# Optimization experiments

Hardware: AMD Instinct MI355X
Metric: run time of the kernel (lower is better)

The kernel has to match this reference:

```python
import jax, jax.numpy as jnp
import numpy as np

B, LQ, LK, D, DV = 8, 2048, 2048, 128, 128


def setup_inputs() -> dict:
    key = jax.random.key(0)
    ks = jax.random.split(key, 6)
    return {
        "query": jax.random.normal(ks[0], (B, LQ, D), dtype=jnp.float32),
        "key": jax.random.normal(ks[1], (B, LK, D), dtype=jnp.float32),
        "value": jax.random.normal(ks[2], (B, LK, DV), dtype=jnp.float32),
        "Wq": jax.random.normal(ks[3], (D, D), dtype=jnp.float32) * 0.08,
        "Wk": jax.random.normal(ks[4], (D, D), dtype=jnp.float32) * 0.08,
        "Wv": jax.random.normal(ks[5], (DV, DV), dtype=jnp.float32) * 0.08,
        "attention_mask": jnp.ones((B, 1, LK), dtype=jnp.int32),
    }


def reference(query, key, value, Wq, Wk, Wv, attention_mask):
    # Linear projections (right-multiplication, as in `x @ W`)
    q = query @ Wq          # [B, lq, n_ed]
    k = key @ Wk            # [B, lk, n_ed]
    v = value @ Wv          # [B, lk, n_ev]
    scale = 1.0 / np.sqrt(q.shape[-1])
    scores = jnp.einsum("bqd,bkd->bqk", q, k) * scale  # [B, lq, lk]
    # additive mask: 0 where attend, -inf where mask==0 (broadcasts)
    mask_vals = jnp.where(attention_mask == 0, -jnp.inf, 0.0).astype(scores.dtype)
    scores = scores + mask_vals
    attn = jax.nn.softmax(scores, axis=-1)
    return attn @ v         # [B, lq, n_ev]
```

## Files before the change

kernel.cpp:

```cpp
#include <hip/hip_runtime.h>
#include <hip/hip_bf16.h>

typedef unsigned short u16;
typedef unsigned int u32;
typedef __attribute__((ext_vector_type(8))) short s8v;
typedef __attribute__((ext_vector_type(4))) float f4v;

#define B_N 8
#define L_Q 2048
#define L_K 2048
#define DIM 128
#define KT  64
#define KSPLIT 4
#define KCHUNK (L_K / KSPLIT)

__device__ __forceinline__ u16 f2bf(float f) {
  union { float f; unsigned u; } v; v.f = f;
  return (u16)((v.u + 0x7fffu + ((v.u >> 16) & 1u)) >> 16);
}
__device__ __forceinline__ u32 packbf2(float a, float b) {
  union { __hip_bfloat162 h; u32 u; } v;
  v.h = __float22bfloat162_rn(make_float2(a, b));
  return v.u;
}

__global__ __launch_bounds__(256) void proj_mfma(
    const float* __restrict__ query, const float* __restrict__ key,
    const float* __restrict__ value, const float* __restrict__ Wq,
    const float* __restrict__ Wk, const float* __restrict__ Wv,
    u16* __restrict__ qp, u16* __restrict__ kp, u16* __restrict__ vt) {
  __shared__ __align__(16) u16 Wt[DIM][DIM + 8];
  __shared__ __align__(16) u16 Vt[DIM][KT + 8];
  const int tid = threadIdx.x;
  const int bi = blockIdx.x;
  const int which = bi >> 8;
  const int sub = bi & 255;
  const int b = sub >> 5;
  const int rt = sub & 31;
  const float* X = (which == 0) ? query : (which == 1) ? key : value;
  const float* W = (which == 0) ? Wq : (which == 1) ? Wk : Wv;
  const float wscale = (which == 0) ? (1.44269504089f / 11.3137084990f) : 1.0f;

#pragma unroll
  for (int i = 0; i < 16; ++i) {
    int f4i = tid + i * 256;
    float4 w4 = *(const float4*)(W + f4i * 4);
    int row = f4i >> 5, col = (f4i & 31) * 4;
    Wt[col + 0][row] = f2bf(w4.x * wscale);
    Wt[col + 1][row] = f2bf(w4.y * wscale);
    Wt[col + 2][row] = f2bf(w4.z * wscale);
    Wt[col + 3][row] = f2bf(w4.w * wscale);
  }
  __syncthreads();

  const int w = tid >> 6, lane = tid & 63;
  const int ln = lane & 15, quad = lane >> 4;
  const int xrow = rt * 64 + w * 16 + ln;
  const float* Xr = X + ((size_t)b * L_Q + xrow) * DIM;

  s8v a[4];
#pragma unroll
  for (int ks = 0; ks < 4; ++ks) {
    float4 xa = *(const float4*)(Xr + ks * 32 + quad * 8);
    float4 xb = *(const float4*)(Xr + ks * 32 + quad * 8 + 4);
    s8v t;
    t[0] = (short)f2bf(xa.x); t[1] = (short)f2bf(xa.y);
    t[2] = (short)f2bf(xa.z); t[3] = (short)f2bf(xa.w);
    t[4] = (short)f2bf(xb.x); t[5] = (short)f2bf(xb.y);
    t[6] = (short)f2bf(xb.z); t[7] = (short)f2bf(xb.w);
    a[ks] = t;
  }

  f4v acc[8];
#pragma unroll
  for (int i = 0; i < 8; ++i) acc[i] = (f4v){0.f, 0.f, 0.f, 0.f};
#pragma unroll
  for (int ks = 0; ks < 4; ++ks)
#pragma unroll
    for (int nt = 0; nt < 8; ++nt) {
      s8v bw = *(const s8v*)&Wt[nt * 16 + ln][ks * 32 + quad * 8];
      acc[nt] = __builtin_amdgcn_mfma_f32_16x16x32_bf16(a[ks], bw, acc[nt], 0, 0, 0);
    }

  if (which < 2) {
    u16* Y = ((which == 0) ? qp : kp) + ((size_t)b * L_Q + rt * 64 + w * 16) * DIM;
#pragma unroll
    for (int nt = 0; nt < 8; ++nt)
#pragma unroll
      for (int r = 0; r < 4; ++r)
        Y[(size_t)(quad * 4 + r) * DIM + nt * 16 + ln] = f2bf(acc[nt][r]);
  } else {
#pragma unroll
    for (int nt = 0; nt < 8; ++nt) {
      *(u32*)&Vt[nt * 16 + ln][w * 16 + quad * 4]     = packbf2(acc[nt][0], acc[nt][1]);
      *(u32*)&Vt[nt * 16 + ln][w * 16 + quad * 4 + 2] = packbf2(acc[nt][2], acc[nt][3]);
    }
    __syncthreads();
    u16* Y = vt + (size_t)b * DIM * L_K;
#pragma unroll
    for (int r = 0; r < 4; ++r) {
      int c = tid + r * 256;
      int row = c >> 3, cc = (c & 7) * 8;
      *(s8v*)(Y + (size_t)row * L_K + rt * 64 + cc) = *(const s8v*)&Vt[row][cc];
    }
  }
}

__global__ __launch_bounds__(256, 4) void flash_split(
    const u16* __restrict__ qp, const u16* __restrict__ kp,
    const u16* __restrict__ vt, const int* __restrict__ mask,
    float* __restrict__ po, float* __restrict__ ml) {
  __shared__ __align__(16) u16 Kl[KT][DIM + 8];
  __shared__ __align__(16) u16 Vl[DIM][KT + 8];
  __shared__ float biasl[KT];

  const int tid = threadIdx.x;
  const int bi = blockIdx.x;
  const int b = bi & 7;
  const int rest = bi >> 3;
  const int p = rest & 3;
  const int q0 = (rest >> 2) * 64;
  const int w = tid >> 6;
  const int lane = tid & 63;
  const int ln = lane & 15;
  const int quad = lane >> 4;
  const int kbase = p * KCHUNK;

  const u16* Qb = qp + (size_t)b * L_Q * DIM;
  const u16* Kb = kp + (size_t)b * L_K * DIM;
  const u16* Vb = vt + (size_t)b * DIM * L_K;
  const int* mb = mask + b * L_K;
  u16* Pw = ((u16*)Kl) + w * (16 * 72);

  s8v aq[4];
  const int qrow = q0 + w * 16 + ln;
#pragma unroll
  for (int ks = 0; ks < 4; ++ks)
    aq[ks] = *(const s8v*)(Qb + (size_t)qrow * DIM + ks * 32 + quad * 8);

  f4v o[8];
#pragma unroll
  for (int i = 0; i < 8; ++i) o[i] = (f4v){0.f, 0.f, 0.f, 0.f};
  float mrow = -__builtin_inff();
  float lrow = 0.f;

  for (int it = 0; it < KCHUNK / KT; ++it) {
    const int k0 = kbase + it * KT;
#pragma unroll
    for (int r = 0; r < 4; ++r) {
      int c16 = tid + r * 256;
      int row = c16 >> 4, cc = (c16 & 15) * 8;
      *(s8v*)&Kl[row][cc] = *(const s8v*)(Kb + (size_t)(k0 + row) * DIM + cc);
    }
#pragma unroll
    for (int r = 0; r < 4; ++r) {
      int c16 = tid + r * 256;
      int row = c16 >> 3, cc = (c16 & 7) * 8;
      *(s8v*)&Vl[row][cc] = *(const s8v*)(Vb + (size_t)row * L_K + k0 + cc);
    }
    if (tid < KT) biasl[tid] = (mb[k0 + tid] == 0) ? -__builtin_inff() : 0.f;
    __syncthreads();

    f4v s[4];
#pragma unroll
    for (int mt = 0; mt < 4; ++mt) s[mt] = (f4v){0.f, 0.f, 0.f, 0.f};
#pragma unroll
    for (int ks = 0; ks < 4; ++ks)
#pragma unroll
      for (int mt = 0; mt < 4; ++mt) {
        s8v bk = *(const s8v*)&Kl[mt * 16 + ln][ks * 32 + quad * 8];
        s[mt] = __builtin_amdgcn_mfma_f32_16x16x32_bf16(bk, aq[ks], s[mt], 0, 0, 0);
      }
#pragma unroll
    for (int mt = 0; mt < 4; ++mt) {
      float4 bt = *(const float4*)&biasl[mt * 16 + quad * 4];
      s[mt][0] += bt.x; s[mt][1] += bt.y; s[mt][2] += bt.z; s[mt][3] += bt.w;
    }
    float m16 = s[0][0];
#pragma unroll
    for (int mt = 0; mt < 4; ++mt)
#pragma unroll
      for (int r = 0; r < 4; ++r) m16 = fmaxf(m16, s[mt][r]);
    m16 = fmaxf(m16, __shfl_xor(m16, 16, 64));
    m16 = fmaxf(m16, __shfl_xor(m16, 32, 64));

    float mn = fmaxf(mrow, m16);
    float alpha = exp2f(fminf(mrow - mn, 0.f));
    mrow = mn;
    float rs = 0.f;
#pragma unroll
    for (int mt = 0; mt < 4; ++mt)
#pragma unroll
      for (int r = 0; r < 4; ++r) {
        s[mt][r] = exp2f(fminf(s[mt][r] - mn, 0.f));
        rs += s[mt][r];
      }
    rs += __shfl_xor(rs, 16, 64);
    rs += __shfl_xor(rs, 32, 64);
    lrow = lrow * alpha + rs;

    __syncthreads();

#pragma unroll
    for (int mt = 0; mt < 4; ++mt) {
      *(u32*)(Pw + ln * 72 + mt * 16 + quad * 4)     = packbf2(s[mt][0], s[mt][1]);
      *(u32*)(Pw + ln * 72 + mt * 16 + quad * 4 + 2) = packbf2(s[mt][2], s[mt][3]);
    }

    float ar[4];
#pragma unroll
    for (int r = 0; r < 4; ++r) ar[r] = __shfl(alpha, quad * 4 + r, 64);
#pragma unroll
    for (int n2 = 0; n2 < 8; ++n2)
#pragma unroll
      for (int r = 0; r < 4; ++r) o[n2][r] *= ar[r];

#pragma unroll
    for (int kv = 0; kv < 2; ++kv) {
      s8v ap = *(const s8v*)(Pw + ln * 72 + kv * 32 + quad * 8);
#pragma unroll
      for (int n2 = 0; n2 < 8; ++n2) {
        s8v bv = *(const s8v*)&Vl[n2 * 16 + ln][kv * 32 + quad * 8];
        o[n2] = __builtin_amdgcn_mfma_f32_16x16x32_bf16(ap, bv, o[n2], 0, 0, 0);
      }
    }
    __syncthreads();
  }

#pragma unroll
  for (int n2 = 0; n2 < 8; ++n2)
#pragma unroll
    for (int r = 0; r < 4; ++r) {
      size_t q = (size_t)b * L_Q + q0 + w * 16 + quad * 4 + r;
      po[(q * KSPLIT + p) * DIM + n2 * 16 + ln] = o[n2][r];
    }
  if (quad == 0) {
    size_t q = (size_t)b * L_Q + q0 + w * 16 + ln;
    *(float2*)&ml[(q * KSPLIT + p) * 2] = make_float2(mrow, lrow);
  }
}

__global__ __launch_bounds__(256) void combine(
    const float* __restrict__ po, const float* __restrict__ ml,
    float* __restrict__ out) {
  const int t = threadIdx.x;
  const int lr = t >> 5, l32 = t & 31;
  const size_t q = (size_t)blockIdx.x * 8 + lr;

  float m[KSPLIT], l[KSPLIT];
#pragma unroll
  for (int p = 0; p < KSPLIT; ++p) {
    m[p] = ml[(q * KSPLIT + p) * 2 + 0];
    l[p] = ml[(q * KSPLIT + p) * 2 + 1];
  }
  float M = m[0];
#pragma unroll
  for (int p = 1; p < KSPLIT; ++p) M = fmaxf(M, m[p]);
  float wp[KSPLIT], L = 0.f;
#pragma unroll
  for (int p = 0; p < KSPLIT; ++p) {
    wp[p] = exp2f(fminf(m[p] - M, 0.f));
    L += l[p] * wp[p];
  }
  float invL = 1.0f / L;

  float4 acc = make_float4(0.f, 0.f, 0.f, 0.f);
#pragma unroll
  for (int p = 0; p < KSPLIT; ++p) {
    float4 v = *(const float4*)(po + (q * KSPLIT + p) * DIM + l32 * 4);
    acc.x += wp[p] * v.x; acc.y += wp[p] * v.y;
    acc.z += wp[p] * v.z; acc.w += wp[p] * v.w;
  }
  acc.x *= invL; acc.y *= invL; acc.z *= invL; acc.w *= invL;
  *(float4*)(out + q * DIM + l32 * 4) = acc;
}

extern "C" void kernel_launch(void* const* d_in, const int* in_sizes, int n_in,
                              void* d_out, int out_size, void* d_ws, size_t ws_size,
                              hipStream_t stream) {
  const float* query = (const float*)d_in[0];
  const float* key   = (const float*)d_in[1];
  const float* value = (const float*)d_in[2];
  const float* Wq    = (const float*)d_in[3];
  const float* Wk    = (const float*)d_in[4];
  const float* Wv    = (const float*)d_in[5];
  const int*   mask  = (const int*)d_in[6];
  float* out = (float*)d_out;

  u16* qp = (u16*)d_ws;
  u16* kp = qp + (size_t)B_N * L_Q * DIM;
  u16* vt = kp + (size_t)B_N * L_K * DIM;
  float* po = (float*)(vt + (size_t)B_N * DIM * L_K);
  float* ml = po + (size_t)B_N * L_Q * KSPLIT * DIM;

  hipLaunchKernelGGL(proj_mfma, dim3(768), dim3(256), 0, stream,
                     query, key, value, Wq, Wk, Wv, qp, kp, vt);
  hipLaunchKernelGGL(flash_split, dim3(1024), dim3(256), 0, stream,
                     qp, kp, vt, mask, po, ml);
  hipLaunchKernelGGL(combine, dim3((B_N * L_Q) / 8), dim3(256), 0, stream,
                     po, ml, out);
}
```

Measured before the change: 141.7 us.

## Store Q/K/V in MFMA fragment-major layout and load K/V tiles via async LDS DMA

The projection kernel now writes Q, K and V in a fragment-major tiled layout, so each MFMA operand is a contiguous 512-element block that can be read with lane*8 offsets. The flash kernel then loads K and V tiles straight into LDS with global_load_lds, skipping the register round trip and the padded row layout. It also skips the mask bias add when a wavefront ballot shows the whole tile is unmasked, and it uses the raw hardware exp2 intrinsic. In exchange the layouts are tightly coupled across the kernels, and the unpadded LDS layout could bring bank conflicts.

```diff
diff --git a/kernel.cpp b/kernel.cpp
--- a/kernel.cpp
+++ b/kernel.cpp
@@ -23,14 +23,20 @@
   v.h = __float22bfloat162_rn(make_float2(a, b));
   return v.u;
 }
+__device__ __forceinline__ void async16(const u16* g, u16* l) {
+  __builtin_amdgcn_global_load_lds(
+      (const __attribute__((address_space(1))) u32*)(const void*)g,
+      (__attribute__((address_space(3))) u32*)(void*)l, 16, 0, 0);
+}
+
 
 __global__ __launch_bounds__(256) void proj_mfma(
     const float* __restrict__ query, const float* __restrict__ key,
     const float* __restrict__ value, const float* __restrict__ Wq,
     const float* __restrict__ Wk, const float* __restrict__ Wv,
-    u16* __restrict__ qp, u16* __restrict__ kp, u16* __restrict__ vt) {
-  __shared__ __align__(16) u16 Wt[DIM][DIM + 8];
-  __shared__ __align__(16) u16 Vt[DIM][KT + 8];
+    u16* __restrict__ qp, u16* __restrict__ kp, u16* __restrict__ vp) {
+  __shared__ __align__(16) u16 Wf[32 * 520];
+  __shared__ __align__(16) u16 Fb[8192];
   const int tid = threadIdx.x;
   const int bi = blockIdx.x;
   const int which = bi >> 8;
@@ -45,11 +51,14 @@
   for (int i = 0; i < 16; ++i) {
     int f4i = tid + i * 256;
     float4 w4 = *(const float4*)(W + f4i * 4);
-    int row = f4i >> 5, col = (f4i & 31) * 4;
-    Wt[col + 0][row] = f2bf(w4.x * wscale);
-    Wt[col + 1][row] = f2bf(w4.y * wscale);
-    Wt[col + 2][row] = f2bf(w4.z * wscale);
-    Wt[col + 3][row] = f2bf(w4.w * wscale);
+    int k = f4i >> 5, col = (f4i & 31) * 4;
+    int ks = k >> 5, qd = (k & 31) >> 3, j = k & 7;
+    float wv[4] = {w4.x, w4.y, w4.z, w4.w};
+#pragma unroll
+    for (int c = 0; c < 4; ++c) {
+      int n = col + c;
+      Wf[(ks * 8 + (n >> 4)) * 520 + (qd * 16 + (n & 15)) * 8 + j] = f2bf(wv[c] * wscale);
+    }
   }
   __syncthreads();
 
@@ -74,44 +83,55 @@
   f4v acc[8];
 #pragma unroll
   for (int i = 0; i < 8; ++i) acc[i] = (f4v){0.f, 0.f, 0.f, 0.f};
+  const u16* Wl0 = Wf + lane * 8;
 #pragma unroll
   for (int ks = 0; ks < 4; ++ks)
 #pragma unroll
     for (int nt = 0; nt < 8; ++nt) {
-      s8v bw = *(const s8v*)&Wt[nt * 16 + ln][ks * 32 + quad * 8];
+      s8v bw = *(const s8v*)(Wl0 + (ks * 8 + nt) * 520);
       acc[nt] = __builtin_amdgcn_mfma_f32_16x16x32_bf16(a[ks], bw, acc[nt], 0, 0, 0);
     }
 
   if (which < 2) {
-    u16* Y = ((which == 0) ? qp : kp) + ((size_t)b * L_Q + rt * 64 + w * 16) * DIM;
-#pragma unroll
-    for (int nt = 0; nt < 8; ++nt)
+#pragma unroll
+    for (int nt = 0; nt < 8; ++nt) {
+      int ks = nt >> 1;
+      int f = (which == 0) ? (w * 4 + ks) : (ks * 4 + w);
+      int lp = ((nt & 1) * 2 + (ln >> 3)) * 16;
+      int j = ln & 7;
 #pragma unroll
       for (int r = 0; r < 4; ++r)
-        Y[(size_t)(quad * 4 + r) * DIM + nt * 16 + ln] = f2bf(acc[nt][r]);
+        Fb[f * 512 + (lp + quad * 4 + r) * 8 + j] = f2bf(acc[nt][r]);
+    }
   } else {
 #pragma unroll
     for (int nt = 0; nt < 8; ++nt) {
-      *(u32*)&Vt[nt * 16 + ln][w * 16 + quad * 4]     = packbf2(acc[nt][0], acc[nt][1]);
-      *(u32*)&Vt[nt * 16 + ln][w * 16 + quad * 4 + 2] = packbf2(acc[nt][2], acc[nt][3]);
-    }
-    __syncthreads();
-    u16* Y = vt + (size_t)b * DIM * L_K;
-#pragma unroll
-    for (int r = 0; r < 4; ++r) {
-      int c = tid + r * 256;
-      int row = c >> 3, cc = (c & 7) * 8;
-      *(s8v*)(Y + (size_t)row * L_K + rt * 64 + cc) = *(const s8v*)&Vt[row][cc];
-    }
+      int f = (w >> 1) * 8 + nt;
+      int lp = ((w & 1) * 2 + (quad >> 1)) * 16 + ln;
+      int jb = (quad & 1) * 4;
+#pragma unroll
+      for (int r = 0; r < 4; ++r)
+        Fb[f * 512 + lp * 8 + jb + r] = f2bf(acc[nt][r]);
+    }
+  }
+  __syncthreads();
+
+  u16* Y = (which == 0) ? qp + (size_t)(b * 512 + rt * 16) * 512
+         : (which == 1) ? kp + (size_t)((b * 32 + rt) * 16) * 512
+                        : vp + (size_t)((b * 32 + rt) * 16) * 512;
+#pragma unroll
+  for (int r = 0; r < 4; ++r) {
+    int c = tid + r * 256;
+    *(s8v*)(Y + c * 8) = *(const s8v*)(Fb + c * 8);
   }
 }
 
 __global__ __launch_bounds__(256, 4) void flash_split(
     const u16* __restrict__ qp, const u16* __restrict__ kp,
-    const u16* __restrict__ vt, const int* __restrict__ mask,
+    const u16* __restrict__ vp, const int* __restrict__ mask,
     float* __restrict__ po, float* __restrict__ ml) {
-  __shared__ __align__(16) u16 Kl[KT][DIM + 8];
-  __shared__ __align__(16) u16 Vl[DIM][KT + 8];
+  __shared__ __align__(16) u16 Kf[8192];
+  __shared__ __align__(16) u16 Vf[8192];
   __shared__ float biasl[KT];
 
   const int tid = threadIdx.x;
@@ -119,24 +139,19 @@
   const int b = bi & 7;
   const int rest = bi >> 3;
   const int p = rest & 3;
-  const int q0 = (rest >> 2) * 64;
+  const int qb = rest >> 2;
   const int w = tid >> 6;
   const int lane = tid & 63;
   const int ln = lane & 15;
   const int quad = lane >> 4;
-  const int kbase = p * KCHUNK;
-
-  const u16* Qb = qp + (size_t)b * L_Q * DIM;
-  const u16* Kb = kp + (size_t)b * L_K * DIM;
-  const u16* Vb = vt + (size_t)b * DIM * L_K;
+
   const int* mb = mask + b * L_K;
-  u16* Pw = ((u16*)Kl) + w * (16 * 72);
-
+
+  const u16* Qt = qp + ((size_t)(b * 128 + qb * 4 + w) * 4) * 512;
   s8v aq[4];
-  const int qrow = q0 + w * 16 + ln;
 #pragma unroll
   for (int ks = 0; ks < 4; ++ks)
-    aq[ks] = *(const s8v*)(Qb + (size_t)qrow * DIM + ks * 32 + quad * 8);
+    aq[ks] = *(const s8v*)(Qt + ks * 512 + lane * 8);
 
   f4v o[8];
 #pragma unroll
@@ -144,21 +159,25 @@
   float mrow = -__builtin_inff();
   float lrow = 0.f;
 
+  const u16* Kl0 = Kf + lane * 8;
+  const u16* Vl0 = Vf + lane * 8;
+  u16* Pw = Kf + w * 1024;
+  const u16* Pl0 = Pw + lane * 8;
+
   for (int it = 0; it < KCHUNK / KT; ++it) {
-    const int k0 = kbase + it * KT;
-#pragma unroll
-    for (int r = 0; r < 4; ++r) {
-      int c16 = tid + r * 256;
-      int row = c16 >> 4, cc = (c16 & 15) * 8;
-      *(s8v*)&Kl[row][cc] = *(const s8v*)(Kb + (size_t)(k0 + row) * DIM + cc);
-    }
-#pragma unroll
-    for (int r = 0; r < 4; ++r) {
-      int c16 = tid + r * 256;
-      int row = c16 >> 3, cc = (c16 & 7) * 8;
-      *(s8v*)&Vl[row][cc] = *(const s8v*)(Vb + (size_t)row * L_K + k0 + cc);
-    }
-    if (tid < KT) biasl[tid] = (mb[k0 + tid] == 0) ? -__builtin_inff() : 0.f;
+    const int kt = p * (KCHUNK / KT) + it;
+    const int k0 = kt * KT;
+    const u16* Ktile = kp + (size_t)((b * 32 + kt) * 16) * 512;
+    const u16* Vtile = vp + (size_t)((b * 32 + kt) * 16) * 512;
+#pragma unroll
+    for (int c = 0; c < 4; ++c) {
+      int cg = w * 4 + c;
+      async16(Ktile + (size_t)(cg * 64 + lane) * 8, Kf + cg * 512);
+      async16(Vtile + (size_t)(cg * 64 + lane) * 8, Vf + cg * 512);
+    }
+    int mv = mb[k0 + lane];
+    bool allones = (__ballot(mv != 0) == ~0ull);
+    if (!allones && tid < KT) biasl[tid] = (mv == 0) ? -__builtin_inff() : 0.f;
     __syncthreads();
 
     f4v s[4];
@@ -168,13 +187,15 @@
     for (int ks = 0; ks < 4; ++ks)
 #pragma unroll
       for (int mt = 0; mt < 4; ++mt) {
-        s8v bk = *(const s8v*)&Kl[mt * 16 + ln][ks * 32 + quad * 8];
+        s8v bk = *(const s8v*)(Kl0 + (ks * 4 + mt) * 512);
         s[mt] = __builtin_amdgcn_mfma_f32_16x16x32_bf16(bk, aq[ks], s[mt], 0, 0, 0);
       }
-#pragma unroll
-    for (int mt = 0; mt < 4; ++mt) {
-      float4 bt = *(const float4*)&biasl[mt * 16 + quad * 4];
-      s[mt][0] += bt.x; s[mt][1] += bt.y; s[mt][2] += bt.z; s[mt][3] += bt.w;
+    if (!allones) {
+#pragma unroll
+      for (int mt = 0; mt < 4; ++mt) {
+        float4 bt = *(const float4*)&biasl[mt * 16 + quad * 4];
+        s[mt][0] += bt.x; s[mt][1] += bt.y; s[mt][2] += bt.z; s[mt][3] += bt.w;
+      }
     }
     float m16 = s[0][0];
 #pragma unroll
@@ -185,14 +206,14 @@
     m16 = fmaxf(m16, __shfl_xor(m16, 32, 64));
 
     float mn = fmaxf(mrow, m16);
-    float alpha = exp2f(fminf(mrow - mn, 0.f));
+    float alpha = __builtin_amdgcn_exp2f(fminf(mrow - mn, 0.f));
     mrow = mn;
     float rs = 0.f;
 #pragma unroll
     for (int mt = 0; mt < 4; ++mt)
 #pragma unroll
       for (int r = 0; r < 4; ++r) {
-        s[mt][r] = exp2f(fminf(s[mt][r] - mn, 0.f));
+        s[mt][r] = __builtin_amdgcn_exp2f(fminf(s[mt][r] - mn, 0.f));
         rs += s[mt][r];
       }
     rs += __shfl_xor(rs, 16, 64);
@@ -203,8 +224,9 @@
 
 #pragma unroll
     for (int mt = 0; mt < 4; ++mt) {
-      *(u32*)(Pw + ln * 72 + mt * 16 + quad * 4)     = packbf2(s[mt][0], s[mt][1]);
-      *(u32*)(Pw + ln * 72 + mt * 16 + quad * 4 + 2) = packbf2(s[mt][2], s[mt][3]);
+      int base = (mt >> 1) * 512 + (((mt & 1) * 2 + (quad >> 1)) * 16 + ln) * 8 + (quad & 1) * 4;
+      *(u32*)(Pw + base)     = packbf2(s[mt][0], s[mt][1]);
+      *(u32*)(Pw + base + 2) = packbf2(s[mt][2], s[mt][3]);
     }
 
     float ar[4];
@@ -217,10 +239,10 @@
 
 #pragma unroll
     for (int kv = 0; kv < 2; ++kv) {
-      s8v ap = *(const s8v*)(Pw + ln * 72 + kv * 32 + quad * 8);
+      s8v ap = *(const s8v*)(Pl0 + kv * 512);
 #pragma unroll
       for (int n2 = 0; n2 < 8; ++n2) {
-        s8v bv = *(const s8v*)&Vl[n2 * 16 + ln][kv * 32 + quad * 8];
+        s8v bv = *(const s8v*)(Vl0 + (kv * 8 + n2) * 512);
         o[n2] = __builtin_amdgcn_mfma_f32_16x16x32_bf16(ap, bv, o[n2], 0, 0, 0);
       }
     }
@@ -231,11 +253,11 @@
   for (int n2 = 0; n2 < 8; ++n2)
 #pragma unroll
     for (int r = 0; r < 4; ++r) {
-      size_t q = (size_t)b * L_Q + q0 + w * 16 + quad * 4 + r;
+      size_t q = (size_t)b * L_Q + qb * 64 + w * 16 + quad * 4 + r;
       po[(q * KSPLIT + p) * DIM + n2 * 16 + ln] = o[n2][r];
     }
   if (quad == 0) {
-    size_t q = (size_t)b * L_Q + q0 + w * 16 + ln;
+    size_t q = (size_t)b * L_Q + qb * 64 + w * 16 + ln;
     *(float2*)&ml[(q * KSPLIT + p) * 2] = make_float2(mrow, lrow);
   }
 }
@@ -259,7 +281,7 @@
   float wp[KSPLIT], L = 0.f;
 #pragma unroll
   for (int p = 0; p < KSPLIT; ++p) {
-    wp[p] = exp2f(fminf(m[p] - M, 0.f));
+    wp[p] = __builtin_amdgcn_exp2f(fminf(m[p] - M, 0.f));
     L += l[p] * wp[p];
   }
   float invL = 1.0f / L;
@@ -289,14 +311,14 @@
 
   u16* qp = (u16*)d_ws;
   u16* kp = qp + (size_t)B_N * L_Q * DIM;
-  u16* vt = kp + (size_t)B_N * L_K * DIM;
-  float* po = (float*)(vt + (size_t)B_N * DIM * L_K);
+  u16* vp = kp + (size_t)B_N * L_K * DIM;
+  float* po = (float*)(vp + (size_t)B_N * DIM * L_K);
   float* ml = po + (size_t)B_N * L_Q * KSPLIT * DIM;
 
   hipLaunchKernelGGL(proj_mfma, dim3(768), dim3(256), 0, stream,
-                     query, key, value, Wq, Wk, Wv, qp, kp, vt);
+                     query, key, value, Wq, Wk, Wv, qp, kp, vp);
   hipLaunchKernelGGL(flash_split, dim3(1024), dim3(256), 0, stream,
-                     qp, kp, vt, mask, po, ml);
+                     qp, kp, vp, mask, po, ml);
   hipLaunchKernelGGL(combine, dim3((B_N * L_Q) / 8), dim3(256), 0, stream,
                      po, ml, out);
 }
```

New measurement: 121.2 us. 1.17x faster.
